# Kernel optimization log

Hardware: AMD Instinct MI355X
Metric: run time of the kernel (lower is better)

The kernel has to match this reference:

```python
import jax, jax.numpy as jnp
import numpy as np

FDS = [80, 160, 400, 600]
N, E, G, IN = 20000, 320000, 128, 3072
EPS = 1e-5  # BatchNorm1d default eps


def setup_inputs():
    key = jax.random.key(0)
    ks = iter(jax.random.split(key, 64))
    inp = {}
    inp["x"] = jax.random.normal(next(ks), (N, IN), jnp.float32)
    inp["edge_index"] = jax.random.randint(next(ks), (2, E), 0, N)
    inp["batch"] = jnp.sort(jax.random.randint(next(ks), (N,), 0, G))
    for i, fd in enumerate(FDS):
        din = IN if i == 0 else FDS[i - 1]
        def u(shape, fan):
            s = 1.0 / np.sqrt(fan)
            return jax.random.uniform(next(ks), shape, jnp.float32, -s, s)
        inp[f"wa{i}"] = u((din, 4 * fd), din)      # Linear(din, 4*fd)
        inp[f"ba{i}"] = u((4 * fd,), din)
        inp[f"wb{i}"] = u((4 * fd, fd), 4 * fd)    # Linear(4*fd, fd)
        inp[f"bb{i}"] = u((fd,), 4 * fd)
        inp[f"gw{i}"] = u((fd, fd), fd)            # GCNConv weight
        inp[f"gb{i}"] = jnp.zeros((fd,), jnp.float32)  # GCNConv bias
        inp[f"gamma{i}"] = jnp.ones((fd,), jnp.float32)
        inp[f"beta{i}"] = jnp.zeros((fd,), jnp.float32)
        inp[f"mean{i}"] = jax.random.normal(next(ks), (fd,), jnp.float32) * 0.1
        inp[f"var{i}"] = jax.random.uniform(next(ks), (fd,), jnp.float32, 0.5, 1.5)
    return inp


def _gcn_edges(edge_index, n):
    # GCNConv default: add self-loops, symmetric D^-1/2 (A+I) D^-1/2 normalization
    loops = jnp.arange(n)
    src = jnp.concatenate([edge_index[0], loops])
    dst = jnp.concatenate([edge_index[1], loops])
    deg = jax.ops.segment_sum(jnp.ones(src.shape, jnp.float32), dst, num_segments=n)
    dinv = jnp.where(deg > 0, jax.lax.rsqrt(deg), 0.0)
    return src, dst, dinv[src] * dinv[dst]


def _forward(x, edge_index, batch, params):
    src, dst, norm = _gcn_edges(edge_index, N)
    for (wa, ba, wb, bb, gw, gb, gamma, beta, mean, var) in params:
        h = jax.nn.relu(x @ wa + ba)   # dropout = identity in eval mode
        h = jax.nn.relu(h @ wb + bb)
        h = h @ gw                     # GCN linear transform
        # gather -> normalize -> scatter-add message passing, then bias
        h = jax.ops.segment_sum(h[src] * norm[:, None], dst, num_segments=N) + gb
        # BatchNorm1d (eval: running stats)
        h = (h - mean) * jax.lax.rsqrt(var + EPS) * gamma + beta
        x = jax.nn.relu(h)             # residual branch is dead: dims never match
    return jax.ops.segment_max(x, batch, num_segments=G)  # global_max_pool


def reference(x, edge_index, batch,
              wa0, ba0, wb0, bb0, gw0, gb0, gamma0, beta0, mean0, var0,
              wa1, ba1, wb1, bb1, gw1, gb1, gamma1, beta1, mean1, var1,
              wa2, ba2, wb2, bb2, gw2, gb2, gamma2, beta2, mean2, var2,
              wa3, ba3, wb3, bb3, gw3, gb3, gamma3, beta3, mean3, var3):
    params = [
        (wa0, ba0, wb0, bb0, gw0, gb0, gamma0, beta0, mean0, var0),
        (wa1, ba1, wb1, bb1, gw1, gb1, gamma1, beta1, mean1, var1),
        (wa2, ba2, wb2, bb2, gw2, gb2, gamma2, beta2, mean2, var2),
        (wa3, ba3, wb3, bb3, gw3, gb3, gamma3, beta3, mean3, var3),
    ]
    return _forward(x, edge_index, batch, params)
```

## Files before the change

### kernel.cpp

```cpp
#include <hip/hip_runtime.h>
#include <cstdint>
#include <cstddef>
#include <cmath>


#define EPS_BN 1e-5f

typedef unsigned short u16;
typedef short short8 __attribute__((ext_vector_type(8)));
typedef u16 u16x8 __attribute__((ext_vector_type(8)));
typedef u16 u16x4 __attribute__((ext_vector_type(4)));
typedef float fx4 __attribute__((ext_vector_type(4)));

__device__ __forceinline__ u16 bf16_rn(float f) {
  unsigned u = __float_as_uint(f);
  return (u16)((u + 0x7FFFu + ((u >> 16) & 1u)) >> 16);
}
__device__ __forceinline__ float bf16_f(u16 h) {
  return __uint_as_float(((unsigned)h) << 16);
}

__device__ __forceinline__ void gload16(const void* g, void* l) {
  __builtin_amdgcn_global_load_lds(
      (const __attribute__((address_space(1))) void*)g,
      (__attribute__((address_space(3))) void*)l, 16, 0, 0);
}

__device__ __forceinline__ void map_tile(int b, int tm, int tn, int T,
                                         int& mt, int& nt) {
  const int x = b & 7;
  const int s = b >> 3;
  const int cap = ((tm - x + 7) >> 3) * tn;
  if (s < cap) {
    const int q = s / tn;
    mt = x + (q << 3);
    nt = s - q * tn;
    return;
  }
  int r = s - cap;
  for (int xp = 0; xp < x; ++xp) {
    const int nbp = (T - xp + 7) >> 3;
    const int capp = ((tm - xp + 7) >> 3) * tn;
    if (nbp > capp) r += nbp - capp;
  }
  for (int xq = 0; xq < 8; ++xq) {
    const int nbq = (T - xq + 7) >> 3;
    const int capq = ((tm - xq + 7) >> 3) * tn;
    const int def = capq - nbq;
    if (def > 0) {
      if (r < def) {
        const int sq = nbq + r;
        const int q = sq / tn;
        mt = xq + (q << 3);
        nt = sq - q * tn;
        return;
      }
      r -= def;
    }
  }
  mt = 0; nt = 0;
}

template <int OUTMODE, bool SPLITA>
__global__ __launch_bounds__(256, 2) void gemm_mfma(
    const u16* __restrict__ Ahi, const u16* __restrict__ Alo,
    const float* __restrict__ Af,
    const u16* __restrict__ Bhi, const u16* __restrict__ Blo,
    const float* __restrict__ bias,
    float* __restrict__ Cf, u16* __restrict__ Chi, u16* __restrict__ Clo,
    int M, int N, int K, int lda, int ldb, int ldc, int tm, int tn) {
  __shared__ __align__(16) u16 As[2][2][128 * 32];
  __shared__ __align__(16) u16 Bs[2][2][128 * 32];

  int mt, nt;
  map_tile(blockIdx.x, tm, tn, tm * tn, mt, nt);
  const int m0 = mt * 128;
  const int n0 = nt * 128;

  const int tid = threadIdx.x;
  const int lane = tid & 63;
  const int wid = tid >> 6;
  const int wm = (wid >> 1) * 64;
  const int wn = (wid & 1) * 64;
  const int quad = lane >> 4;
  const int l15 = lane & 15;

  const int srow = tid >> 2;
  const int sg = ((tid & 3) ^ srow) & 3;
  int ar0 = m0 + srow;      if (ar0 >= M) ar0 = M - 1;
  int ar1 = m0 + srow + 64; if (ar1 >= M) ar1 = M - 1;
  int br0 = n0 + srow;      if (br0 >= N) br0 = N - 1;
  int br1 = n0 + srow + 64; if (br1 >= N) br1 = N - 1;
  const size_t aof0 = (size_t)ar0 * lda + (sg << 3);
  const size_t aof1 = (size_t)ar1 * lda + (sg << 3);
  const size_t bof0 = (size_t)br0 * ldb + (sg << 3);
  const size_t bof1 = (size_t)br1 * ldb + (sg << 3);
  const int l0 = wid << 9;
  const int l1 = 2048 + (wid << 9);
  const int wls = srow * 32 + ((tid & 3) << 3);

  fx4 zf = {0.f, 0.f, 0.f, 0.f};
  fx4 acc[4][4];
#pragma unroll
  for (int a = 0; a < 4; ++a)
#pragma unroll
    for (int b = 0; b < 4; ++b) acc[a][b] = zf;

  const int nk = (K + 31) >> 5;

  if (SPLITA) {
    gload16(Bhi + bof0, &Bs[0][0][l0]);
    gload16(Bhi + bof1, &Bs[0][0][l1]);
    gload16(Blo + bof0, &Bs[0][1][l0]);
    gload16(Blo + bof1, &Bs[0][1][l1]);
#pragma unroll
    for (int it = 0; it < 2; ++it) {
      const float* pp = Af + (it ? aof1 : aof0);
      const fx4 f0 = *(const fx4*)pp;
      const fx4 f1 = *(const fx4*)(pp + 4);
      u16x8 h, l;
#pragma unroll
      for (int j = 0; j < 4; ++j) {
        const u16 hb = bf16_rn(f0[j]);
        h[j] = hb;
        l[j] = bf16_rn(f0[j] - bf16_f(hb));
      }
#pragma unroll
      for (int j = 0; j < 4; ++j) {
        const u16 hb = bf16_rn(f1[j]);
        h[4 + j] = hb;
        l[4 + j] = bf16_rn(f1[j] - bf16_f(hb));
      }
      *(u16x8*)&As[0][0][wls + it * 2048] = h;
      *(u16x8*)&As[0][1][wls + it * 2048] = l;
    }
  } else {
    gload16(Ahi + aof0, &As[0][0][l0]);
    gload16(Ahi + aof1, &As[0][0][l1]);
    gload16(Alo + aof0, &As[0][1][l0]);
    gload16(Alo + aof1, &As[0][1][l1]);
    gload16(Bhi + bof0, &Bs[0][0][l0]);
    gload16(Bhi + bof1, &Bs[0][0][l1]);
    gload16(Blo + bof0, &Bs[0][1][l0]);
    gload16(Blo + bof1, &Bs[0][1][l1]);
  }

  for (int ki = 0; ki < nk; ++ki) {
    const int cur = ki & 1;
    __syncthreads();

    const bool pre = (ki + 1) < nk;
    const int kn = (ki + 1) << 5;
    fx4 pA0 = zf, pA1 = zf, pA2 = zf, pA3 = zf;
    if (pre) {
      if (SPLITA) {
        gload16(Bhi + bof0 + kn, &Bs[cur ^ 1][0][l0]);
        gload16(Bhi + bof1 + kn, &Bs[cur ^ 1][0][l1]);
        gload16(Blo + bof0 + kn, &Bs[cur ^ 1][1][l0]);
        gload16(Blo + bof1 + kn, &Bs[cur ^ 1][1][l1]);
        const float* pp0 = Af + aof0 + kn;
        const float* pp1 = Af + aof1 + kn;
        pA0 = *(const fx4*)pp0;
        pA1 = *(const fx4*)(pp0 + 4);
        pA2 = *(const fx4*)pp1;
        pA3 = *(const fx4*)(pp1 + 4);
      } else {
        gload16(Ahi + aof0 + kn, &As[cur ^ 1][0][l0]);
        gload16(Ahi + aof1 + kn, &As[cur ^ 1][0][l1]);
        gload16(Alo + aof0 + kn, &As[cur ^ 1][1][l0]);
        gload16(Alo + aof1 + kn, &As[cur ^ 1][1][l1]);
        gload16(Bhi + bof0 + kn, &Bs[cur ^ 1][0][l0]);
        gload16(Bhi + bof1 + kn, &Bs[cur ^ 1][0][l1]);
        gload16(Blo + bof0 + kn, &Bs[cur ^ 1][1][l0]);
        gload16(Blo + bof1 + kn, &Bs[cur ^ 1][1][l1]);
      }
    }

    short8 ah[4], al[4], bh[4], bl[4];
#pragma unroll
    for (int t = 0; t < 4; ++t) {
      const int rA = wm + t * 16 + l15;
      const int oa = rA * 32 + (((quad ^ rA) & 3) << 3);
      ah[t] = *(const short8*)&As[cur][0][oa];
      al[t] = *(const short8*)&As[cur][1][oa];
      const int rB = wn + t * 16 + l15;
      const int ob = rB * 32 + (((quad ^ rB) & 3) << 3);
      bh[t] = *(const short8*)&Bs[cur][0][ob];
      bl[t] = *(const short8*)&Bs[cur][1][ob];
    }
#pragma unroll
    for (int a = 0; a < 4; ++a)
#pragma unroll
      for (int b = 0; b < 4; ++b) {
        acc[a][b] = __builtin_amdgcn_mfma_f32_16x16x32_bf16(ah[a], bh[b], acc[a][b], 0, 0, 0);
        acc[a][b] = __builtin_amdgcn_mfma_f32_16x16x32_bf16(ah[a], bl[b], acc[a][b], 0, 0, 0);
        acc[a][b] = __builtin_amdgcn_mfma_f32_16x16x32_bf16(al[a], bh[b], acc[a][b], 0, 0, 0);
      }

    if (SPLITA && pre) {
      u16x8 h0, l0v, h1, l1v;
#pragma unroll
      for (int j = 0; j < 4; ++j) {
        u16 hb = bf16_rn(pA0[j]);
        h0[j] = hb;
        l0v[j] = bf16_rn(pA0[j] - bf16_f(hb));
      }
#pragma unroll
      for (int j = 0; j < 4; ++j) {
        u16 hb = bf16_rn(pA1[j]);
        h0[4 + j] = hb;
        l0v[4 + j] = bf16_rn(pA1[j] - bf16_f(hb));
      }
#pragma unroll
      for (int j = 0; j < 4; ++j) {
        u16 hb = bf16_rn(pA2[j]);
        h1[j] = hb;
        l1v[j] = bf16_rn(pA2[j] - bf16_f(hb));
      }
#pragma unroll
      for (int j = 0; j < 4; ++j) {
        u16 hb = bf16_rn(pA3[j]);
        h1[4 + j] = hb;
        l1v[4 + j] = bf16_rn(pA3[j] - bf16_f(hb));
      }
      const int nb = cur ^ 1;
      *(u16x8*)&As[nb][0][wls] = h0;
      *(u16x8*)&As[nb][1][wls] = l0v;
      *(u16x8*)&As[nb][0][wls + 2048] = h1;
      *(u16x8*)&As[nb][1][wls + 2048] = l1v;
    }
  }

#pragma unroll
  for (int a = 0; a < 4; ++a)
#pragma unroll
    for (int b = 0; b < 4; ++b) {
      const int gn = n0 + wn + b * 16 + l15;
      if (gn >= ldc) continue;
      const bool live = gn < N;
      const float bv = (OUTMODE == 1 && live) ? bias[gn] : 0.f;
#pragma unroll
      for (int r = 0; r < 4; ++r) {
        const int gm = m0 + wm + a * 16 + quad * 4 + r;
        if (gm >= M) continue;
        float v = live ? acc[a][b][r] : 0.f;
        if (OUTMODE == 1) {
          v = live ? fmaxf(v + bv, 0.f) : 0.f;
          const u16 hb = bf16_rn(v);
          Chi[(size_t)gm * ldc + gn] = hb;
          Clo[(size_t)gm * ldc + gn] = bf16_rn(v - bf16_f(hb));
        } else {
          Cf[(size_t)gm * ldc + gn] = v;
        }
      }
    }
}

struct TSJob { const float* W; u16* Th; u16* Tl; int K; int Kp; int N; int tiles_k; int base; };
struct TSJobs { TSJob j[12]; };

__global__ __launch_bounds__(256) void transpose_split_all(TSJobs jobs, int njobs) {
  const int b = blockIdx.x;
  int ji = 0;
  while (ji + 1 < njobs && jobs.j[ji + 1].base <= b) ++ji;
  const TSJob J = jobs.j[ji];
  const int t = b - J.base;
  const int k0 = (t % J.tiles_k) * 32;
  const int n0 = (t / J.tiles_k) * 32;
  __shared__ float tile[32][33];
  const int tx = threadIdx.x & 31, ty = threadIdx.x >> 5;
#pragma unroll
  for (int i = 0; i < 32; i += 8) {
    const int k = k0 + ty + i, n = n0 + tx;
    tile[ty + i][tx] = (k < J.K && n < J.N) ? J.W[(size_t)k * J.N + n] : 0.f;
  }
  __syncthreads();
#pragma unroll
  for (int i = 0; i < 32; i += 8) {
    const int n = n0 + ty + i, k = k0 + tx;
    if (n < J.N && k < J.Kp) {
      const float f = tile[tx][ty + i];
      const u16 hb = bf16_rn(f);
      J.Th[(size_t)n * J.Kp + k] = hb;
      J.Tl[(size_t)n * J.Kp + k] = bf16_rn(f - bf16_f(hb));
    }
  }
}

__global__ void count_deg(const int* __restrict__ dst, int E, int* __restrict__ cnt) {
  int e = blockIdx.x * blockDim.x + threadIdx.x;
  if (e < E) atomicAdd(&cnt[dst[e]], 1);
}

__global__ void compute_dinv(const int* __restrict__ cnt, float* __restrict__ dinv, int N) {
  int i = blockIdx.x * blockDim.x + threadIdx.x;
  if (i < N) dinv[i] = rsqrtf((float)(cnt[i] + 1));
}

__global__ void scan_block(const int* __restrict__ cnt, int* __restrict__ partial,
                           int* __restrict__ blocksum, int N) {
  __shared__ int s[256];
  const int t = threadIdx.x;
  const int i = blockIdx.x * 256 + t;
  int v = (i < N) ? cnt[i] : 0;
  s[t] = v;
  __syncthreads();
  for (int off = 1; off < 256; off <<= 1) {
    int u = (t >= off) ? s[t - off] : 0;
    __syncthreads();
    s[t] += u;
    __syncthreads();
  }
  if (i < N) partial[i] = s[t];
  if (t == 255) blocksum[blockIdx.x] = s[255];
}

__global__ void scan_sums(int* __restrict__ blocksum, int NB) {
  __shared__ int s[256];
  const int t = threadIdx.x;
  int v = (t < NB) ? blocksum[t] : 0;
  s[t] = v;
  __syncthreads();
  for (int off = 1; off < 256; off <<= 1) {
    int u = (t >= off) ? s[t - off] : 0;
    __syncthreads();
    s[t] += u;
    __syncthreads();
  }
  if (t < NB) blocksum[t] = s[t] - v;
}

__global__ void finalize_rowptr(const int* __restrict__ partial, const int* __restrict__ blockoff,
                                int* __restrict__ rowptr, int N) {
  int i = blockIdx.x * 256 + threadIdx.x;
  if (i < N) rowptr[i + 1] = partial[i] + blockoff[blockIdx.x];
  if (i == 0) rowptr[0] = 0;
}

__global__ void fill_csr(const int* __restrict__ src, const int* __restrict__ dst, int E,
                         const int* __restrict__ rowptr, int* __restrict__ cursor,
                         int* __restrict__ colidx) {
  int e = blockIdx.x * blockDim.x + threadIdx.x;
  if (e < E) {
    int d = dst[e];
    int p = atomicAdd(&cursor[d], 1);
    colidx[rowptr[d] + p] = src[e];
  }
}

__global__ void mp_bn_relu(
    const float* __restrict__ H, const int* __restrict__ rowptr,
    const int* __restrict__ colidx, const float* __restrict__ dinv,
    const float* __restrict__ gb, const float* __restrict__ gamma,
    const float* __restrict__ beta, const float* __restrict__ mean,
    const float* __restrict__ var,
    u16* __restrict__ Xh, u16* __restrict__ Xl, int N, int F, int Fp) {
  const int nch = Fp >> 2;
  const int idx = blockIdx.x * blockDim.x + threadIdx.x;
  if (idx >= N * nch) return;
  const int i = idx / nch;
  const int c = idx - i * nch;
  const size_t rowi = (size_t)i * Fp + (c << 2);
  if ((c << 2) >= F) {
    const u16x4 z = {0, 0, 0, 0};
    *(u16x4*)(Xh + rowi) = z;
    *(u16x4*)(Xl + rowi) = z;
    return;
  }
  const float di = dinv[i];
  fx4 acc = (di * di) * *(const fx4*)(H + rowi);
  const int e0 = rowptr[i], e1 = rowptr[i + 1];
  int e = e0;
  for (; e + 4 <= e1; e += 4) {
    const int s0 = colidx[e + 0], s1 = colidx[e + 1];
    const int s2 = colidx[e + 2], s3 = colidx[e + 3];
    const float w0 = di * dinv[s0], w1 = di * dinv[s1];
    const float w2 = di * dinv[s2], w3 = di * dinv[s3];
    const fx4 v0 = *(const fx4*)(H + (size_t)s0 * Fp + (c << 2));
    const fx4 v1 = *(const fx4*)(H + (size_t)s1 * Fp + (c << 2));
    const fx4 v2 = *(const fx4*)(H + (size_t)s2 * Fp + (c << 2));
    const fx4 v3 = *(const fx4*)(H + (size_t)s3 * Fp + (c << 2));
    acc += w0 * v0;
    acc += w1 * v1;
    acc += w2 * v2;
    acc += w3 * v3;
  }
  for (; e < e1; ++e) {
    const int s = colidx[e];
    acc += (di * dinv[s]) * *(const fx4*)(H + (size_t)s * Fp + (c << 2));
  }
  u16x4 oh, ol;
#pragma unroll
  for (int j = 0; j < 4; ++j) {
    const int col = (c << 2) + j;
    float v = (acc[j] + gb[col] - mean[col]) * rsqrtf(var[col] + EPS_BN) * gamma[col] + beta[col];
    v = fmaxf(v, 0.f);
    const u16 hb = bf16_rn(v);
    oh[j] = hb;
    ol[j] = bf16_rn(v - bf16_f(hb));
  }
  *(u16x4*)(Xh + rowi) = oh;
  *(u16x4*)(Xl + rowi) = ol;
}

__global__ void pool_seg(const u16* __restrict__ Xh, const u16* __restrict__ Xl,
                         const int* __restrict__ batch, float* __restrict__ out,
                         int N, int F, int ldx) {
  const int g = blockIdx.x;
  int lo = 0, hi = N;
  while (lo < hi) { int m = (lo + hi) >> 1; if (batch[m] < g) lo = m + 1; else hi = m; }
  const int s0 = lo;
  hi = N;
  while (lo < hi) { int m = (lo + hi) >> 1; if (batch[m] <= g) lo = m + 1; else hi = m; }
  const int s1 = lo;
  const int c = threadIdx.x;
  if (c * 4 >= F) return;
  fx4 mx = {-INFINITY, -INFINITY, -INFINITY, -INFINITY};
  for (int i = s0; i < s1; ++i) {
    const size_t off = (size_t)i * ldx + (c << 2);
    const u16x4 h = *(const u16x4*)(Xh + off);
    const u16x4 l = *(const u16x4*)(Xl + off);
#pragma unroll
    for (int j = 0; j < 4; ++j) mx[j] = fmaxf(mx[j], bf16_f(h[j]) + bf16_f(l[j]));
  }
  *(fx4*)(out + (size_t)g * F + (c << 2)) = mx;
}

extern "C" void kernel_launch(void* const* d_in, const int* in_sizes, int n_in,
                              void* d_out, int out_size, void* d_ws, size_t ws_size,
                              hipStream_t stream) {
  const float* x = (const float*)d_in[0];
  const int* edges = (const int*)d_in[1];
  const int* batch = (const int*)d_in[2];
  const int E = in_sizes[1] / 2;
  const int Nn = in_sizes[2];

  static const int FDS[4]  = {80, 160, 400, 600};
  static const int FDP[4]  = {96, 160, 416, 608};
  static const int DINS[4] = {3072, 80, 160, 400};
  static const int DINP[4] = {3072, 96, 160, 416};
  const float *wa[4], *ba[4], *wb[4], *bb[4], *gw[4], *gb[4], *gamma[4], *beta[4], *mean[4], *var[4];
  for (int i = 0; i < 4; ++i) {
    const int b = 3 + 10 * i;
    wa[i] = (const float*)d_in[b + 0];
    ba[i] = (const float*)d_in[b + 1];
    wb[i] = (const float*)d_in[b + 2];
    bb[i] = (const float*)d_in[b + 3];
    gw[i] = (const float*)d_in[b + 4];
    gb[i] = (const float*)d_in[b + 5];
    gamma[i] = (const float*)d_in[b + 6];
    beta[i] = (const float*)d_in[b + 7];
    mean[i] = (const float*)d_in[b + 8];
    var[i] = (const float*)d_in[b + 9];
  }

  char* p = (char*)d_ws;
  auto alloc = [&](size_t bytes) {
    char* r = p;
    p += (bytes + 255) & ~(size_t)255;
    return r;
  };
  u16* actA_h = (u16*)alloc((size_t)Nn * 2400 * 2);
  u16* actA_l = (u16*)alloc((size_t)Nn * 2400 * 2);
  u16* actB_h = (u16*)alloc((size_t)Nn * 608 * 2);
  u16* actB_l = (u16*)alloc((size_t)Nn * 608 * 2);
  float* H3 = (float*)actA_h;

  u16 *waT_h[4], *waT_l[4], *wbT_h[4], *wbT_l[4], *gwT_h[4], *gwT_l[4];
  for (int i = 0; i < 4; ++i) {
    const size_t s1 = (size_t)4 * FDS[i] * DINP[i];
    const size_t s2 = (size_t)FDS[i] * 4 * FDS[i];
    const size_t s3 = (size_t)FDS[i] * FDP[i];
    waT_h[i] = (u16*)alloc(s1 * 2);
    waT_l[i] = (u16*)alloc(s1 * 2);
    wbT_h[i] = (u16*)alloc(s2 * 2);
    wbT_l[i] = (u16*)alloc(s2 * 2);
    gwT_h[i] = (u16*)alloc(s3 * 2);
    gwT_l[i] = (u16*)alloc(s3 * 2);
  }

  int* cnt = (int*)alloc((size_t)Nn * sizeof(int));
  int* cursor = (int*)alloc((size_t)Nn * sizeof(int));
  int* partial = (int*)alloc((size_t)Nn * sizeof(int));
  int* blocksum = (int*)alloc(256 * sizeof(int));
  int* rowptr = (int*)alloc((size_t)(Nn + 1) * sizeof(int));
  int* colidx = (int*)alloc((size_t)E * sizeof(int));
  float* dinv = (float*)alloc((size_t)Nn * sizeof(float));

  const int* srcIdx = edges;
  const int* dstIdx = edges + E;

  {
    TSJobs jobs;
    int base = 0, ji = 0;
    auto addjob = [&](const float* W, int K, int Kp, int Ncols, u16* Th, u16* Tl) {
      const int tk = Kp / 32, tn = (Ncols + 31) / 32;
      jobs.j[ji++] = TSJob{W, Th, Tl, K, Kp, Ncols, tk, base};
      base += tk * tn;
    };
    for (int i = 0; i < 4; ++i) {
      addjob(wa[i], DINS[i], DINP[i], 4 * FDS[i], waT_h[i], waT_l[i]);
      addjob(wb[i], 4 * FDS[i], 4 * FDS[i], FDS[i], wbT_h[i], wbT_l[i]);
      addjob(gw[i], FDS[i], FDP[i], FDS[i], gwT_h[i], gwT_l[i]);
    }
    transpose_split_all<<<base, 256, 0, stream>>>(jobs, 12);
  }

  hipMemsetAsync(cnt, 0, (size_t)Nn * sizeof(int), stream);
  hipMemsetAsync(cursor, 0, (size_t)Nn * sizeof(int), stream);

  const int EB = (E + 255) / 256;
  const int NB = (Nn + 255) / 256;
  count_deg<<<EB, 256, 0, stream>>>(dstIdx, E, cnt);
  compute_dinv<<<NB, 256, 0, stream>>>(cnt, dinv, Nn);
  scan_block<<<NB, 256, 0, stream>>>(cnt, partial, blocksum, Nn);
  scan_sums<<<1, 256, 0, stream>>>(blocksum, NB);
  finalize_rowptr<<<NB, 256, 0, stream>>>(partial, blocksum, rowptr, Nn);
  fill_csr<<<EB, 256, 0, stream>>>(srcIdx, dstIdx, E, rowptr, cursor, colidx);

  const int tm = (Nn + 127) / 128;
  for (int i = 0; i < 4; ++i) {
    const int fd = FDS[i], fdp = FDP[i];
    const int hid = 4 * fd;
    const int din = DINS[i], dinp = DINP[i];

    {
      const int tn = (hid + 127) / 128;
      if (i == 0) {
        gemm_mfma<1, true><<<tm * tn, 256, 0, stream>>>(
            nullptr, nullptr, x, waT_h[0], waT_l[0], ba[0],
            nullptr, actA_h, actA_l, Nn, hid, din, din, dinp, hid, tm, tn);
      } else {
        gemm_mfma<1, false><<<tm * tn, 256, 0, stream>>>(
            actB_h, actB_l, nullptr, waT_h[i], waT_l[i], ba[i],
            nullptr, actA_h, actA_l, Nn, hid, din, dinp, dinp, hid, tm, tn);
      }
    }
    {
      const int tn = (fd + 127) / 128;
      gemm_mfma<1, false><<<tm * tn, 256, 0, stream>>>(
          actA_h, actA_l, nullptr, wbT_h[i], wbT_l[i], bb[i],
          nullptr, actB_h, actB_l, Nn, fd, hid, hid, hid, fdp, tm, tn);
    }
    {
      const int tn = (fd + 127) / 128;
      gemm_mfma<0, false><<<tm * tn, 256, 0, stream>>>(
          actB_h, actB_l, nullptr, gwT_h[i], gwT_l[i], nullptr,
          H3, nullptr, nullptr, Nn, fd, fd, fdp, fdp, fdp, tm, tn);
    }
    {
      const int items = Nn * (fdp >> 2);
      mp_bn_relu<<<(items + 255) / 256, 256, 0, stream>>>(
          H3, rowptr, colidx, dinv, gb[i], gamma[i], beta[i], mean[i], var[i],
          actB_h, actB_l, Nn, fd, fdp);
    }
  }

  pool_seg<<<out_size / 600, 192, 0, stream>>>(actB_h, actB_l, batch, (float*)d_out,
                                               Nn, 600, 608);
}
```

Measured before the change: 1.797 ms.

## Prefetch GEMM tiles two k-steps ahead with explicit vmcnt waits

Restructures the GEMM main loop so global loads for tile k+2 are issued after the compute of tile k, with a prologue that preloads two stages. The implicit full-drain __syncthreads is replaced with explicit s_waitcnt vmcnt(8)/lgkmcnt and raw s_barrier, so one stage of loads stays in flight across the barrier. This aims to hide global memory latency behind MFMA work. It relies on hand-counted outstanding-load numbers (8 per stage), which may be wrong for the SPLITA path where A uses register loads, risking races or overly conservative waits.

```diff
diff --git a/kernel.cpp b/kernel.cpp
--- a/kernel.cpp
+++ b/kernel.cpp
@@ -108,32 +108,48 @@
 
   const int nk = (K + 31) >> 5;
 
+  fx4 pA0 = zf, pA1 = zf, pA2 = zf, pA3 = zf;
+
   if (SPLITA) {
+    const fx4 t0 = *(const fx4*)(Af + aof0);
+    const fx4 t1 = *(const fx4*)(Af + aof0 + 4);
+    const fx4 t2 = *(const fx4*)(Af + aof1);
+    const fx4 t3 = *(const fx4*)(Af + aof1 + 4);
     gload16(Bhi + bof0, &Bs[0][0][l0]);
     gload16(Bhi + bof1, &Bs[0][0][l1]);
     gload16(Blo + bof0, &Bs[0][1][l0]);
     gload16(Blo + bof1, &Bs[0][1][l1]);
-#pragma unroll
-    for (int it = 0; it < 2; ++it) {
-      const float* pp = Af + (it ? aof1 : aof0);
-      const fx4 f0 = *(const fx4*)pp;
-      const fx4 f1 = *(const fx4*)(pp + 4);
-      u16x8 h, l;
-#pragma unroll
-      for (int j = 0; j < 4; ++j) {
-        const u16 hb = bf16_rn(f0[j]);
-        h[j] = hb;
-        l[j] = bf16_rn(f0[j] - bf16_f(hb));
-      }
-#pragma unroll
-      for (int j = 0; j < 4; ++j) {
-        const u16 hb = bf16_rn(f1[j]);
-        h[4 + j] = hb;
-        l[4 + j] = bf16_rn(f1[j] - bf16_f(hb));
-      }
-      *(u16x8*)&As[0][0][wls + it * 2048] = h;
-      *(u16x8*)&As[0][1][wls + it * 2048] = l;
-    }
+    if (nk > 1) {
+      gload16(Bhi + bof0 + 32, &Bs[1][0][l0]);
+      gload16(Bhi + bof1 + 32, &Bs[1][0][l1]);
+      gload16(Blo + bof0 + 32, &Bs[1][1][l0]);
+      gload16(Blo + bof1 + 32, &Bs[1][1][l1]);
+      pA0 = *(const fx4*)(Af + aof0 + 32);
+      pA1 = *(const fx4*)(Af + aof0 + 36);
+      pA2 = *(const fx4*)(Af + aof1 + 32);
+      pA3 = *(const fx4*)(Af + aof1 + 36);
+    }
+    u16x8 h0, lo0, h1, lo1;
+#pragma unroll
+    for (int j = 0; j < 4; ++j) {
+      u16 hb = bf16_rn(t0[j]); h0[j] = hb; lo0[j] = bf16_rn(t0[j] - bf16_f(hb));
+    }
+#pragma unroll
+    for (int j = 0; j < 4; ++j) {
+      u16 hb = bf16_rn(t1[j]); h0[4 + j] = hb; lo0[4 + j] = bf16_rn(t1[j] - bf16_f(hb));
+    }
+#pragma unroll
+    for (int j = 0; j < 4; ++j) {
+      u16 hb = bf16_rn(t2[j]); h1[j] = hb; lo1[j] = bf16_rn(t2[j] - bf16_f(hb));
+    }
+#pragma unroll
+    for (int j = 0; j < 4; ++j) {
+      u16 hb = bf16_rn(t3[j]); h1[4 + j] = hb; lo1[4 + j] = bf16_rn(t3[j] - bf16_f(hb));
+    }
+    *(u16x8*)&As[0][0][wls] = h0;
+    *(u16x8*)&As[0][1][wls] = lo0;
+    *(u16x8*)&As[0][0][wls + 2048] = h1;
+    *(u16x8*)&As[0][1][wls + 2048] = lo1;
   } else {
     gload16(Ahi + aof0, &As[0][0][l0]);
     gload16(Ahi + aof1, &As[0][0][l1]);
@@ -143,38 +159,24 @@
     gload16(Bhi + bof1, &Bs[0][0][l1]);
     gload16(Blo + bof0, &Bs[0][1][l0]);
     gload16(Blo + bof1, &Bs[0][1][l1]);
+    if (nk > 1) {
+      gload16(Ahi + aof0 + 32, &As[1][0][l0]);
+      gload16(Ahi + aof1 + 32, &As[1][0][l1]);
+      gload16(Alo + aof0 + 32, &As[1][1][l0]);
+      gload16(Alo + aof1 + 32, &As[1][1][l1]);
+      gload16(Bhi + bof0 + 32, &Bs[1][0][l0]);
+      gload16(Bhi + bof1 + 32, &Bs[1][0][l1]);
+      gload16(Blo + bof0 + 32, &Bs[1][1][l0]);
+      gload16(Blo + bof1 + 32, &Bs[1][1][l1]);
+    }
   }
 
   for (int ki = 0; ki < nk; ++ki) {
     const int cur = ki & 1;
-    __syncthreads();
-
-    const bool pre = (ki + 1) < nk;
-    const int kn = (ki + 1) << 5;
-    fx4 pA0 = zf, pA1 = zf, pA2 = zf, pA3 = zf;
-    if (pre) {
-      if (SPLITA) {
-        gload16(Bhi + bof0 + kn, &Bs[cur ^ 1][0][l0]);
-        gload16(Bhi + bof1 + kn, &Bs[cur ^ 1][0][l1]);
-        gload16(Blo + bof0 + kn, &Bs[cur ^ 1][1][l0]);
-        gload16(Blo + bof1 + kn, &Bs[cur ^ 1][1][l1]);
-        const float* pp0 = Af + aof0 + kn;
-        const float* pp1 = Af + aof1 + kn;
-        pA0 = *(const fx4*)pp0;
-        pA1 = *(const fx4*)(pp0 + 4);
-        pA2 = *(const fx4*)pp1;
-        pA3 = *(const fx4*)(pp1 + 4);
-      } else {
-        gload16(Ahi + aof0 + kn, &As[cur ^ 1][0][l0]);
-        gload16(Ahi + aof1 + kn, &As[cur ^ 1][0][l1]);
-        gload16(Alo + aof0 + kn, &As[cur ^ 1][1][l0]);
-        gload16(Alo + aof1 + kn, &As[cur ^ 1][1][l1]);
-        gload16(Bhi + bof0 + kn, &Bs[cur ^ 1][0][l0]);
-        gload16(Bhi + bof1 + kn, &Bs[cur ^ 1][0][l1]);
-        gload16(Blo + bof0 + kn, &Bs[cur ^ 1][1][l0]);
-        gload16(Blo + bof1 + kn, &Bs[cur ^ 1][1][l1]);
-      }
-    }
+    if (SPLITA) asm volatile("s_waitcnt lgkmcnt(0)" ::: "memory");
+    if (ki + 1 < nk) asm volatile("s_waitcnt vmcnt(8)" ::: "memory");
+    else             asm volatile("s_waitcnt vmcnt(0)" ::: "memory");
+    __builtin_amdgcn_s_barrier();
 
     short8 ah[4], al[4], bh[4], bl[4];
 #pragma unroll
@@ -197,37 +199,54 @@
         acc[a][b] = __builtin_amdgcn_mfma_f32_16x16x32_bf16(al[a], bh[b], acc[a][b], 0, 0, 0);
       }
 
-    if (SPLITA && pre) {
-      u16x8 h0, l0v, h1, l1v;
+    if (SPLITA && (ki + 1 < nk)) {
+      u16x8 h0, lo0, h1, lo1;
 #pragma unroll
       for (int j = 0; j < 4; ++j) {
-        u16 hb = bf16_rn(pA0[j]);
-        h0[j] = hb;
-        l0v[j] = bf16_rn(pA0[j] - bf16_f(hb));
+        u16 hb = bf16_rn(pA0[j]); h0[j] = hb; lo0[j] = bf16_rn(pA0[j] - bf16_f(hb));
       }
 #pragma unroll
       for (int j = 0; j < 4; ++j) {
-        u16 hb = bf16_rn(pA1[j]);
-        h0[4 + j] = hb;
-        l0v[4 + j] = bf16_rn(pA1[j] - bf16_f(hb));
+        u16 hb = bf16_rn(pA1[j]); h0[4 + j] = hb; lo0[4 + j] = bf16_rn(pA1[j] - bf16_f(hb));
       }
 #pragma unroll
       for (int j = 0; j < 4; ++j) {
-        u16 hb = bf16_rn(pA2[j]);
-        h1[j] = hb;
-        l1v[j] = bf16_rn(pA2[j] - bf16_f(hb));
+        u16 hb = bf16_rn(pA2[j]); h1[j] = hb; lo1[j] = bf16_rn(pA2[j] - bf16_f(hb));
       }
 #pragma unroll
       for (int j = 0; j < 4; ++j) {
-        u16 hb = bf16_rn(pA3[j]);
-        h1[4 + j] = hb;
-        l1v[4 + j] = bf16_rn(pA3[j] - bf16_f(hb));
+        u16 hb = bf16_rn(pA3[j]); h1[4 + j] = hb; lo1[4 + j] = bf16_rn(pA3[j] - bf16_f(hb));
       }
       const int nb = cur ^ 1;
       *(u16x8*)&As[nb][0][wls] = h0;
-      *(u16x8*)&As[nb][1][wls] = l0v;
+      *(u16x8*)&As[nb][1][wls] = lo0;
       *(u16x8*)&As[nb][0][wls + 2048] = h1;
-      *(u16x8*)&As[nb][1][wls + 2048] = l1v;
+      *(u16x8*)&As[nb][1][wls + 2048] = lo1;
+    }
+
+    __builtin_amdgcn_s_barrier();
+
+    if (ki + 2 < nk) {
+      const size_t kn2 = (size_t)(ki + 2) << 5;
+      if (SPLITA) {
+        gload16(Bhi + bof0 + kn2, &Bs[cur][0][l0]);
+        gload16(Bhi + bof1 + kn2, &Bs[cur][0][l1]);
+        gload16(Blo + bof0 + kn2, &Bs[cur][1][l0]);
+        gload16(Blo + bof1 + kn2, &Bs[cur][1][l1]);
+        pA0 = *(const fx4*)(Af + aof0 + kn2);
+        pA1 = *(const fx4*)(Af + aof0 + kn2 + 4);
+        pA2 = *(const fx4*)(Af + aof1 + kn2);
+        pA3 = *(const fx4*)(Af + aof1 + kn2 + 4);
+      } else {
+        gload16(Ahi + aof0 + kn2, &As[cur][0][l0]);
+        gload16(Ahi + aof1 + kn2, &As[cur][0][l1]);
+        gload16(Alo + aof0 + kn2, &As[cur][1][l0]);
+        gload16(Alo + aof1 + kn2, &As[cur][1][l1]);
+        gload16(Bhi + bof0 + kn2, &Bs[cur][0][l0]);
+        gload16(Bhi + bof1 + kn2, &Bs[cur][0][l1]);
+        gload16(Blo + bof0 + kn2, &Bs[cur][1][l0]);
+        gload16(Blo + bof1 + kn2, &Bs[cur][1][l1]);
+      }
     }
   }
 
```

Measured after the change: 1.784 ms. Within noise of the previous version (-0.7%).
